# Kernel tuning notes

Hardware: AMD Instinct MI355X
Metric: run time of the kernel (lower is better)

Reference implementation:

```python
import jax, jax.numpy as jnp
import numpy as np


def setup_inputs() -> dict:
    key = jax.random.key(0)
    k_x, k_pos, k_val, k_temp = jax.random.split(key, 4)
    B, T, D, N = 8, 2048, 512, 4096
    x = jax.random.normal(k_x, (B, T, D), dtype=jnp.float32)
    # module init: positions ~ N(0,1)*0.5, values ~ N(0,1)*0.02
    positions = jax.random.normal(k_pos, (N, D), dtype=jnp.float32) * 0.5
    values = jax.random.normal(k_val, (N, D), dtype=jnp.float32) * 0.02
    # 'trained' temperatures ~ U[4,6] so the RBF kernel does not underflow at D=512
    temperature = 4.0 + 2.0 * jax.random.uniform(k_temp, (N,), dtype=jnp.float32)
    # neuron_scale buffer at late-tide level (MAX_SCALE = 0.8)
    neuron_scale = jnp.full((N,), 0.8, dtype=jnp.float32)
    return {"x": x, "positions": positions, "values": values,
            "temperature": temperature, "neuron_scale": neuron_scale}


def reference(x, positions, values, temperature, neuron_scale):
    B, T, D = x.shape
    x_flat = x.reshape(-1, D)                                  # [M, D], M = B*T
    x_sq = jnp.sum(x_flat * x_flat, axis=-1, keepdims=True)    # [M, 1]
    p_sq = jnp.sum(positions * positions, axis=-1)             # [N]
    cross = x_flat @ positions.T                               # [M, N] GEMM
    dists = jnp.sqrt(jnp.maximum(x_sq + p_sq[None, :] - 2.0 * cross, 0.0))
    effective_temp = (jnp.abs(temperature) + 0.1) * neuron_scale  # [N]
    weights = jnp.exp(-dists / effective_temp[None, :])        # [M, N]
    weights = weights / (jnp.sum(weights, axis=-1, keepdims=True) + 1e-8)
    out = weights @ values                                     # [M, D] GEMM
    return out.reshape(B, T, D)
```

## Files before the change

kernel.cpp:

```cpp
#include <hip/hip_runtime.h>
#include <hip/hip_bf16.h>

typedef __attribute__((ext_vector_type(8))) short short8;
typedef __attribute__((ext_vector_type(4))) float f32x4;
typedef __attribute__((ext_vector_type(4))) unsigned short u16x4;

__device__ __forceinline__ unsigned short f2bf(float f) {
  union { float f; unsigned u; } v; v.f = f;
  unsigned r = v.u + 0x7fffu + ((v.u >> 16) & 1u);
  return (unsigned short)(r >> 16);
}

template <int EPI, int WM, int WN, int MI, int BK, int NBUF>
__global__ __launch_bounds__(WM * WN * 64, 4) void rbf_gemm(
    const unsigned short* __restrict__ A, const unsigned short* __restrict__ Bt,
    int Ncols, int K,
    const float* __restrict__ xsq, const float* __restrict__ psq,
    const float* __restrict__ rtemp, unsigned short* __restrict__ Wout,
    float* __restrict__ part, int Mtot, const float* __restrict__ denin,
    float* __restrict__ outp, int row0, int ldOut) {
  constexpr int NT = WM * WN * 64;
  constexpr int BM = WM * MI * 16;
  constexpr int BN = WN * 64;
  constexpr int CH = BK / 8;
  constexpr int CMASK = CH - 1;
  constexpr int AIT = BM * CH / NT;
  constexpr int BIT = BN * CH / NT;
  constexpr int LOADS = AIT + BIT;
  constexpr int KS = BK / 32;
  constexpr int ASZ = BM * BK;
  constexpr int TSZ = (BM + BN) * BK;
  constexpr int BOUNCE = EPI == 1 ? BM * BN * 2 : BM * BN;
  constexpr int SELEMS = NBUF * TSZ > BOUNCE ? NBUF * TSZ : BOUNCE;
  __shared__ __align__(16) unsigned short smem[SELEMS];

  const int t = threadIdx.x;
  const int lane = t & 63, wid = t >> 6;
  const int wm = wid / WN, wn = wid % WN;
  const int lr = lane & 15, lg = lane >> 4;

  const int nbm = gridDim.x / (Ncols / BN);
  const int bm = blockIdx.x % nbm;
  const int bn = blockIdx.x / nbm;

  const unsigned short* Ab = A + (size_t)bm * BM * K;
  const unsigned short* Bb = Bt + (size_t)bn * BN * K;

  const unsigned short* gA[AIT];
  const unsigned short* gB[BIT];
#pragma unroll
  for (int i = 0; i < AIT; ++i) {
    const int idx = i * NT + t;
    const int r = idx / CH, c = idx & CMASK;
    gA[i] = Ab + (size_t)r * K + ((c ^ (r & CMASK)) << 3);
  }
#pragma unroll
  for (int i = 0; i < BIT; ++i) {
    const int idx = i * NT + t;
    const int r = idx / CH, c = idx & CMASK;
    gB[i] = Bb + (size_t)r * K + ((c ^ (r & CMASK)) << 3);
  }
  const int dwave = wid << 9;

  int offA[MI][KS], offB[4][KS];
#pragma unroll
  for (int mi = 0; mi < MI; ++mi) {
    const int ar = wm * (MI * 16) + mi * 16 + lr;
#pragma unroll
    for (int ks = 0; ks < KS; ++ks)
      offA[mi][ks] = ar * BK + ((((ks << 2) | lg) ^ (ar & CMASK)) << 3);
  }
#pragma unroll
  for (int ni = 0; ni < 4; ++ni) {
    const int br = wn * 64 + ni * 16 + lr;
#pragma unroll
    for (int ks = 0; ks < KS; ++ks)
      offB[ni][ks] = ASZ + br * BK + ((((ks << 2) | lg) ^ (br & CMASK)) << 3);
  }

  f32x4 acc[MI][4];
#pragma unroll
  for (int i = 0; i < MI; ++i)
#pragma unroll
    for (int j = 0; j < 4; ++j) acc[i][j] = (f32x4){0.f, 0.f, 0.f, 0.f};

#define STAGE(bo)                                                                      \
  do {                                                                                 \
    _Pragma("unroll")                                                                  \
    for (int i = 0; i < AIT; ++i) {                                                    \
      __builtin_amdgcn_global_load_lds(                                                \
          (const __attribute__((address_space(1))) void*)gA[i],                        \
          (__attribute__((address_space(3))) void*)(smem + (bo) + i * (NT * 8) + dwave), \
          16, 0, 0);                                                                   \
      gA[i] += BK;                                                                     \
    }                                                                                  \
    _Pragma("unroll")                                                                  \
    for (int i = 0; i < BIT; ++i) {                                                    \
      __builtin_amdgcn_global_load_lds(                                                \
          (const __attribute__((address_space(1))) void*)gB[i],                        \
          (__attribute__((address_space(3))) void*)(smem + (bo) + ASZ + i * (NT * 8) + dwave), \
          16, 0, 0);                                                                   \
      gB[i] += BK;                                                                     \
    }                                                                                  \
  } while (0)

  const int nsteps = K / BK;
  STAGE(0);
  unsigned buf = 0;
  for (int s = 0; s < nsteps; ++s) {
    if (s + 1 < nsteps) {
      STAGE(buf ^ TSZ);
      asm volatile("s_waitcnt vmcnt(%0)" :: "i"(LOADS) : "memory");
    } else {
      asm volatile("s_waitcnt vmcnt(0)" ::: "memory");
    }
    __builtin_amdgcn_s_barrier();
    const unsigned short* sb = smem + buf;
    __builtin_amdgcn_s_setprio(1);
#pragma unroll
    for (int ks = 0; ks < KS; ++ks) {
      short8 af[MI], bf[4];
#pragma unroll
      for (int mi = 0; mi < MI; ++mi) af[mi] = *(const short8*)&sb[offA[mi][ks]];
#pragma unroll
      for (int ni = 0; ni < 4; ++ni) bf[ni] = *(const short8*)&sb[offB[ni][ks]];
#pragma unroll
      for (int mi = 0; mi < MI; ++mi)
#pragma unroll
        for (int ni = 0; ni < 4; ++ni)
          acc[mi][ni] = __builtin_amdgcn_mfma_f32_16x16x32_bf16(af[mi], bf[ni],
                                                                acc[mi][ni], 0, 0, 0);
    }
    __builtin_amdgcn_s_setprio(0);
    asm volatile("s_waitcnt lgkmcnt(0)" ::: "memory");
    __builtin_amdgcn_s_barrier();
    buf ^= TSZ;
  }
#undef STAGE

  if (EPI == 0) {
    float ps[4], rt[4];
#pragma unroll
    for (int ni = 0; ni < 4; ++ni) {
      const int col = bn * BN + wn * 64 + ni * 16 + lr;
      ps[ni] = psq[col];
      rt[ni] = rtemp[col];
    }
    float* slice = part + (size_t)(bn * WN + wn) * Mtot;
#pragma unroll
    for (int mi = 0; mi < MI; ++mi) {
#pragma unroll
      for (int j = 0; j < 4; ++j) {
        const int lrow = wm * (MI * 16) + mi * 16 + lg * 4 + j;
        const int grow = row0 + bm * BM + lrow;
        const float xq = xsq[grow];
        float rsv = 0.f;
#pragma unroll
        for (int ni = 0; ni < 4; ++ni) {
          const int lcol = wn * 64 + ni * 16 + lr;
          float d2 = xq + ps[ni] - 2.0f * acc[mi][ni][j];
          float dist = __builtin_amdgcn_sqrtf(fmaxf(d2, 0.0f));
          float w = __builtin_amdgcn_exp2f(-dist * rt[ni]);
          smem[lrow * BN + (((lcol >> 3) ^ (lrow & 7)) << 3) + (lcol & 7)] = f2bf(w);
          rsv += w;
        }
        rsv += __shfl_xor(rsv, 1);
        rsv += __shfl_xor(rsv, 2);
        rsv += __shfl_xor(rsv, 4);
        rsv += __shfl_xor(rsv, 8);
        if (lr == 0) slice[grow] = rsv;
      }
    }
    __syncthreads();
    constexpr int HB = BN / 8;
#pragma unroll
    for (int i = 0; i < BM * BN / 8 / NT; ++i) {
      const int id = i * NT + t;
      const int r = id / HB, h = id % HB;
      short8 v = *(const short8*)&smem[r * BN + ((h ^ (r & 7)) << 3)];
      *(short8*)&Wout[(size_t)(bm * BM + r) * ldOut + bn * BN + h * 8] = v;
    }
  } else {
    float* smemf = (float*)smem;
#pragma unroll
    for (int mi = 0; mi < MI; ++mi)
#pragma unroll
      for (int j = 0; j < 4; ++j) {
        const int lrow = wm * (MI * 16) + mi * 16 + lg * 4 + j;
#pragma unroll
        for (int ni = 0; ni < 4; ++ni) {
          const int lcol = wn * 64 + ni * 16 + lr;
          smemf[lrow * BN + (((lcol >> 2) ^ (lrow & 7)) << 2) + (lcol & 3)] =
              acc[mi][ni][j];
        }
      }
    __syncthreads();
    constexpr int HB4 = BN / 4;
#pragma unroll
    for (int i = 0; i < BM * BN / 4 / NT; ++i) {
      const int id = i * NT + t;
      const int r = id / HB4, h = id % HB4;
      const int grow = row0 + bm * BM + r;
      const float rd = 1.0f / (denin[grow] + 1e-8f);
      f32x4 v = *(const f32x4*)&smemf[r * BN + ((h ^ (r & 7)) << 2)];
      v *= rd;
      __builtin_nontemporal_store(v,
          (f32x4*)&outp[(size_t)grow * ldOut + bn * BN + h * 4]);
    }
  }
}

__global__ void reduce_denom(const float* __restrict__ part, float* __restrict__ denom,
                             int Mtot, int row0, int S) {
  const int m = row0 + blockIdx.x * 128 + threadIdx.x;
  float s = 0.f;
  for (int i = 0; i < S; ++i) s += part[(size_t)i * Mtot + m];
  denom[m] = s;
}

__global__ void prep_rows(const float* __restrict__ in, unsigned short* __restrict__ outb,
                          float* __restrict__ sq, int D) {
  const int row = blockIdx.x;
  const int t = threadIdx.x;
  const float4 v = ((const float4*)(in + (size_t)row * D))[t];
  u16x4 o = {f2bf(v.x), f2bf(v.y), f2bf(v.z), f2bf(v.w)};
  *(u16x4*)(outb + (size_t)row * D + t * 4) = o;
  float s = v.x * v.x + v.y * v.y + v.z * v.z + v.w * v.w;
  for (int off = 32; off; off >>= 1) s += __shfl_xor(s, off);
  __shared__ float ws[16];
  if ((t & 63) == 0) ws[t >> 6] = s;
  __syncthreads();
  if (t == 0) {
    float tot = 0.f;
    const int nw = blockDim.x >> 6;
    for (int i = 0; i < nw; ++i) tot += ws[i];
    sq[row] = tot;
  }
}

__global__ void prep_scale(const float* __restrict__ tmp, const float* __restrict__ sc,
                           float* __restrict__ rtemp, int N) {
  const int i = blockIdx.x * blockDim.x + threadIdx.x;
  if (i < N) rtemp[i] = 1.4426950408889634f / ((fabsf(tmp[i]) + 0.1f) * sc[i]);
}

__global__ void prep_vT(const float* __restrict__ vals, unsigned short* __restrict__ vT,
                        int N, int D) {
  __shared__ float tile[32][33];
  const int nt = blockIdx.x, dt = blockIdx.y;
  const int tx = threadIdx.x, ty = threadIdx.y;
#pragma unroll
  for (int i = 0; i < 4; ++i) {
    int r = nt * 32 + ty + i * 8;
    tile[ty + i * 8][tx] = vals[(size_t)r * D + dt * 32 + tx];
  }
  __syncthreads();
#pragma unroll
  for (int i = 0; i < 4; ++i) {
    int d = dt * 32 + ty + i * 8;
    vT[(size_t)d * N + nt * 32 + tx] = f2bf(tile[tx][ty + i * 8]);
  }
}

extern "C" void kernel_launch(void* const* d_in, const int* in_sizes, int n_in,
                              void* d_out, int out_size, void* d_ws, size_t ws_size,
                              hipStream_t stream) {
  const float* x = (const float*)d_in[0];
  const float* pos = (const float*)d_in[1];
  const float* vals = (const float*)d_in[2];
  const float* temp = (const float*)d_in[3];
  const float* nsc = (const float*)d_in[4];
  float* out = (float*)d_out;

  const int N = in_sizes[3];
  const int D = in_sizes[1] / N;
  const int M = in_sizes[0] / D;
  const int S = 2 * (N / 128);

  char* ws = (char*)d_ws;
  size_t off = 0;
  auto alloc = [&](size_t bytes) {
    void* p = ws + off;
    off = (off + bytes + 255) & ~(size_t)255;
    return p;
  };
  unsigned short* xb = (unsigned short*)alloc((size_t)M * D * 2);
  unsigned short* pb = (unsigned short*)alloc((size_t)N * D * 2);
  unsigned short* vT = (unsigned short*)alloc((size_t)D * N * 2);
  float* xsq = (float*)alloc((size_t)M * 4);
  float* psq = (float*)alloc((size_t)N * 4);
  float* rtemp = (float*)alloc((size_t)N * 4);
  float* denom = (float*)alloc((size_t)M * 4);
  float* part = (float*)alloc((size_t)S * M * 4);

  size_t avail = ws_size > off ? ws_size - off : 0;
  long long mc_ll = (long long)(avail / ((size_t)N * 2));
  int Mc = (int)((mc_ll / 128) * 128);
  if (Mc > M) Mc = M;
  if (Mc < 128) Mc = 128;
  unsigned short* W = (unsigned short*)alloc((size_t)Mc * N * 2);

  prep_rows<<<M, D / 4, 0, stream>>>(x, xb, xsq, D);
  prep_rows<<<N, D / 4, 0, stream>>>(pos, pb, psq, D);
  prep_scale<<<(N + 255) / 256, 256, 0, stream>>>(temp, nsc, rtemp, N);
  dim3 tg(N / 32, D / 32);
  prep_vT<<<tg, dim3(32, 8), 0, stream>>>(vals, vT, N, D);

  for (int row0 = 0; row0 < M; row0 += Mc) {
    const int mc = (M - row0) < Mc ? (M - row0) : Mc;
    const int g1 = (mc / 128) * (N / 128);
    rbf_gemm<0, 4, 2, 2, 64, 2><<<g1, 512, 0, stream>>>(
        xb + (size_t)row0 * D, pb, N, D, xsq, psq, rtemp, W, part, M,
        nullptr, nullptr, row0, N);
    reduce_denom<<<mc / 128, 128, 0, stream>>>(part, denom, M, row0, S);
    const int g2 = (mc / 128) * (D / 256);
    rbf_gemm<1, 2, 4, 4, 64, 2><<<g2, 512, 0, stream>>>(
        W, vT, D, N, nullptr, nullptr, nullptr, nullptr,
        part, M, denom, out, row0, D);
  }
}
```

Measured before the change: 210.3 us.

## Replace first GEMM with 256x256-tile kernel using phased load/MFMA interleave

Adds a dedicated first-GEMM kernel with 256x256 output tiles, 8 waves and a four-phase schedule. Each phase interleaves LDS fragment reads, partial global-to-LDS prefetch of the next K-slice, barriers and MFMA blocks. The larger tile raises arithmetic intensity and the phased prefetch is meant to hide load latency behind MFMA work. In exchange it uses more registers and LDS, which lowers occupancy to 2 blocks per CU and produces fewer, larger blocks. The denominator-partial count and chunk granularity are adjusted to match.

```diff
diff --git a/kernel.cpp b/kernel.cpp
--- a/kernel.cpp
+++ b/kernel.cpp
@@ -11,13 +11,227 @@
   return (unsigned short)(r >> 16);
 }
 
-template <int EPI, int WM, int WN, int MI, int BK, int NBUF>
-__global__ __launch_bounds__(WM * WN * 64, 4) void rbf_gemm(
+#define GLL(src, dst)                                                     \
+  __builtin_amdgcn_global_load_lds(                                       \
+      (const __attribute__((address_space(1))) void*)(src),               \
+      (__attribute__((address_space(3))) void*)(dst), 16, 0, 0)
+#define BAR __builtin_amdgcn_s_barrier()
+#define LGKM0                                                             \
+  do {                                                                    \
+    asm volatile("s_waitcnt lgkmcnt(0)" ::: "memory");                    \
+    __builtin_amdgcn_sched_barrier(0);                                    \
+  } while (0)
+#define VMC(n) asm volatile("s_waitcnt vmcnt(" #n ")" ::: "memory")
+
+__global__ __launch_bounds__(512, 2) void rbf_qk8p(
     const unsigned short* __restrict__ A, const unsigned short* __restrict__ Bt,
     int Ncols, int K,
     const float* __restrict__ xsq, const float* __restrict__ psq,
     const float* __restrict__ rtemp, unsigned short* __restrict__ Wout,
-    float* __restrict__ part, int Mtot, const float* __restrict__ denin,
+    float* __restrict__ part, int Mtot, int row0, int ldOut) {
+  constexpr int BK = 64;
+  constexpr int ASZ = 256 * 64;
+  constexpr int TSZ = 512 * 64;
+  __shared__ __align__(16) unsigned short smem[2 * TSZ];
+
+  const int t = threadIdx.x;
+  const int lane = t & 63, wid = t >> 6;
+  const int wm = wid >> 2, wn = wid & 3;
+  const int lr = lane & 15, lg = lane >> 4;
+
+  const int nbm = gridDim.x / (Ncols >> 8);
+  const int bm = blockIdx.x % nbm;
+  const int bn = blockIdx.x / nbm;
+
+  const unsigned short* Ab = A + (size_t)bm * 256 * K;
+  const unsigned short* Bb = Bt + (size_t)bn * 256 * K;
+
+  const unsigned short* gB[4];
+#pragma unroll
+  for (int h = 0; h < 2; ++h)
+#pragma unroll
+    for (int i = 0; i < 2; ++i) {
+      const int idx = i * 512 + t;
+      const int r = h * 128 + (idx >> 3), c = idx & 7;
+      gB[h * 2 + i] = Bb + (size_t)r * K + ((c ^ (r & 7)) << 3);
+    }
+  const unsigned short* gAq[4];
+  {
+    const int half = t >> 8, rl = (t & 255) >> 3, c = t & 7;
+#pragma unroll
+    for (int q = 0; q < 4; ++q) {
+      const int R = half * 128 + q * 32 + rl;
+      gAq[q] = Ab + (size_t)R * K + ((c ^ (R & 7)) << 3);
+    }
+  }
+  const int dwB = wid << 9;
+  const int abase = ((wid >> 2) << 13) + ((wid & 3) << 9);
+
+#define STB(bo)                                         \
+  do {                                                  \
+    GLL(gB[0], smem + (bo) + ASZ + dwB);                \
+    gB[0] += BK;                                        \
+    GLL(gB[1], smem + (bo) + ASZ + 4096 + dwB);         \
+    gB[1] += BK;                                        \
+    GLL(gB[2], smem + (bo) + ASZ + 8192 + dwB);         \
+    gB[2] += BK;                                        \
+    GLL(gB[3], smem + (bo) + ASZ + 12288 + dwB);        \
+    gB[3] += BK;                                        \
+  } while (0)
+#define STA(bo, q)                                      \
+  do {                                                  \
+    GLL(gAq[q], smem + (bo) + abase + (q) * 2048);      \
+    gAq[q] += BK;                                       \
+  } while (0)
+
+  int offA[8][2], offB[4][2];
+#pragma unroll
+  for (int mi = 0; mi < 8; ++mi) {
+    const int ar = wm * 128 + mi * 16 + lr;
+#pragma unroll
+    for (int ks = 0; ks < 2; ++ks)
+      offA[mi][ks] = ar * 64 + ((((ks << 2) | lg) ^ (ar & 7)) << 3);
+  }
+#pragma unroll
+  for (int ni = 0; ni < 4; ++ni) {
+    const int br = wn * 64 + ni * 16 + lr;
+#pragma unroll
+    for (int ks = 0; ks < 2; ++ks)
+      offB[ni][ks] = ASZ + br * 64 + ((((ks << 2) | lg) ^ (br & 7)) << 3);
+  }
+
+  f32x4 acc[8][4];
+#pragma unroll
+  for (int i = 0; i < 8; ++i)
+#pragma unroll
+    for (int j = 0; j < 4; ++j) acc[i][j] = (f32x4){0.f, 0.f, 0.f, 0.f};
+
+#define PH_READS_A(p)                                   \
+  afr[0][0] = *(const short8*)&sb[offA[2 * (p)][0]];    \
+  afr[0][1] = *(const short8*)&sb[offA[2 * (p)][1]];    \
+  afr[1][0] = *(const short8*)&sb[offA[2 * (p) + 1][0]]; \
+  afr[1][1] = *(const short8*)&sb[offA[2 * (p) + 1][1]];
+#define PH_MFMA(p)                                                            \
+  __builtin_amdgcn_s_setprio(1);                                              \
+  _Pragma("unroll") for (int ks = 0; ks < 2; ++ks)                            \
+  _Pragma("unroll") for (int r = 0; r < 2; ++r)                               \
+  _Pragma("unroll") for (int ni = 0; ni < 4; ++ni)                            \
+      acc[2 * (p) + r][ni] = __builtin_amdgcn_mfma_f32_16x16x32_bf16(         \
+          afr[r][ks], bfr[ni][ks], acc[2 * (p) + r][ni], 0, 0, 0);            \
+  __builtin_amdgcn_s_setprio(0);
+
+  const int nsteps = K / BK;
+  const int last = nsteps - 1;
+  STB(0);
+  STA(0, 0);
+  STA(0, 1);
+  STA(0, 2);
+  STA(0, 3);
+  VMC(2);
+  BAR;
+
+  for (int tt = 0; tt < nsteps; ++tt) {
+    const int bo = (tt & 1) * TSZ, nbo = bo ^ TSZ;
+    const bool st = tt + 1 < nsteps;
+    const unsigned short* sb = smem + bo;
+    short8 bfr[4][2], afr[2][2];
+#pragma unroll
+    for (int ni = 0; ni < 4; ++ni) {
+      bfr[ni][0] = *(const short8*)&sb[offB[ni][0]];
+      bfr[ni][1] = *(const short8*)&sb[offB[ni][1]];
+    }
+    PH_READS_A(0)
+    if (st) STB(nbo);
+    BAR;
+    LGKM0;
+    PH_MFMA(0)
+    BAR;
+    PH_READS_A(1)
+    if (st) {
+      STA(nbo, 0);
+      STA(nbo, 1);
+    }
+    BAR;
+    LGKM0;
+    PH_MFMA(1)
+    if (tt == last) {
+      VMC(1);
+    } else {
+      VMC(7);
+    }
+    BAR;
+    PH_READS_A(2)
+    if (st) STA(nbo, 2);
+    BAR;
+    LGKM0;
+    PH_MFMA(2)
+    if (tt == last) {
+      VMC(0);
+    } else {
+      VMC(7);
+    }
+    BAR;
+    PH_READS_A(3)
+    if (st) STA(nbo, 3);
+    BAR;
+    LGKM0;
+    PH_MFMA(3)
+    if (tt != last) {
+      VMC(2);
+    }
+    BAR;
+  }
+#undef PH_READS_A
+#undef PH_MFMA
+#undef STB
+#undef STA
+
+  float ps[4], rt[4];
+#pragma unroll
+  for (int ni = 0; ni < 4; ++ni) {
+    const int col = bn * 256 + wn * 64 + ni * 16 + lr;
+    ps[ni] = psq[col];
+    rt[ni] = rtemp[col];
+  }
+  float* slice = part + (size_t)(bn * 4 + wn) * Mtot;
+#pragma unroll
+  for (int mi = 0; mi < 8; ++mi) {
+#pragma unroll
+    for (int j = 0; j < 4; ++j) {
+      const int lrow = wm * 128 + mi * 16 + lg * 4 + j;
+      const int grow = row0 + bm * 256 + lrow;
+      const float xq = xsq[grow];
+      float rsv = 0.f;
+#pragma unroll
+      for (int ni = 0; ni < 4; ++ni) {
+        const int lcol = wn * 64 + ni * 16 + lr;
+        float d2 = xq + ps[ni] - 2.0f * acc[mi][ni][j];
+        float dist = __builtin_amdgcn_sqrtf(fmaxf(d2, 0.0f));
+        float w = __builtin_amdgcn_exp2f(-dist * rt[ni]);
+        smem[lrow * 256 + (((lcol >> 3) ^ (lrow & 7)) << 3) + (lcol & 7)] = f2bf(w);
+        rsv += w;
+      }
+      rsv += __shfl_xor(rsv, 1);
+      rsv += __shfl_xor(rsv, 2);
+      rsv += __shfl_xor(rsv, 4);
+      rsv += __shfl_xor(rsv, 8);
+      if (lr == 0) slice[grow] = rsv;
+    }
+  }
+  __syncthreads();
+#pragma unroll
+  for (int i = 0; i < 16; ++i) {
+    const int id = i * 512 + t;
+    const int r = id >> 5, h = id & 31;
+    short8 v = *(const short8*)&smem[r * 256 + ((h ^ (r & 7)) << 3)];
+    *(short8*)&Wout[(size_t)(bm * 256 + r) * ldOut + bn * 256 + h * 8] = v;
+  }
+}
+
+template <int EPI, int WM, int WN, int MI, int BK, int NBUF>
+__global__ __launch_bounds__(WM * WN * 64, 4) void rbf_gemm(
+    const unsigned short* __restrict__ A, const unsigned short* __restrict__ Bt,
+    int Ncols, int K, const float* __restrict__ denin,
     float* __restrict__ outp, int row0, int ldOut) {
   constexpr int NT = WM * WN * 64;
   constexpr int BM = WM * MI * 16;
@@ -30,7 +244,7 @@
   constexpr int KS = BK / 32;
   constexpr int ASZ = BM * BK;
   constexpr int TSZ = (BM + BN) * BK;
-  constexpr int BOUNCE = EPI == 1 ? BM * BN * 2 : BM * BN;
+  constexpr int BOUNCE = BM * BN * 2;
   constexpr int SELEMS = NBUF * TSZ > BOUNCE ? NBUF * TSZ : BOUNCE;
   __shared__ __align__(16) unsigned short smem[SELEMS];
 
@@ -84,24 +298,16 @@
 #pragma unroll
     for (int j = 0; j < 4; ++j) acc[i][j] = (f32x4){0.f, 0.f, 0.f, 0.f};
 
-#define STAGE(bo)                                                                      \
-  do {                                                                                 \
-    _Pragma("unroll")                                                                  \
-    for (int i = 0; i < AIT; ++i) {                                                    \
-      __builtin_amdgcn_global_load_lds(                                                \
-          (const __attribute__((address_space(1))) void*)gA[i],                        \
-          (__attribute__((address_space(3))) void*)(smem + (bo) + i * (NT * 8) + dwave), \
-          16, 0, 0);                                                                   \
-      gA[i] += BK;                                                                     \
-    }                                                                                  \
-    _Pragma("unroll")                                                                  \
-    for (int i = 0; i < BIT; ++i) {                                                    \
-      __builtin_amdgcn_global_load_lds(                                                \
-          (const __attribute__((address_space(1))) void*)gB[i],                        \
-          (__attribute__((address_space(3))) void*)(smem + (bo) + ASZ + i * (NT * 8) + dwave), \
-          16, 0, 0);                                                                   \
-      gB[i] += BK;                                                                     \
-    }                                                                                  \
+#define STAGE(bo)                                                              \
+  do {                                                                         \
+    _Pragma("unroll") for (int i = 0; i < AIT; ++i) {                          \
+      GLL(gA[i], smem + (bo) + i * (NT * 8) + dwave);                          \
+      gA[i] += BK;                                                             \
+    }                                                                          \
+    _Pragma("unroll") for (int i = 0; i < BIT; ++i) {                          \
+      GLL(gB[i], smem + (bo) + ASZ + i * (NT * 8) + dwave);                    \
+      gB[i] += BK;                                                             \
+    }                                                                          \
   } while (0)
 
   const int nsteps = K / BK;
@@ -114,7 +320,7 @@
     } else {
       asm volatile("s_waitcnt vmcnt(0)" ::: "memory");
     }
-    __builtin_amdgcn_s_barrier();
+    BAR;
     const unsigned short* sb = smem + buf;
     __builtin_amdgcn_s_setprio(1);
 #pragma unroll
@@ -133,80 +339,36 @@
     }
     __builtin_amdgcn_s_setprio(0);
     asm volatile("s_waitcnt lgkmcnt(0)" ::: "memory");
-    __builtin_amdgcn_s_barrier();
+    BAR;
     buf ^= TSZ;
   }
 #undef STAGE
 
-  if (EPI == 0) {
-    float ps[4], rt[4];
-#pragma unroll
-    for (int ni = 0; ni < 4; ++ni) {
-      const int col = bn * BN + wn * 64 + ni * 16 + lr;
-      ps[ni] = psq[col];
-      rt[ni] = rtemp[col];
-    }
-    float* slice = part + (size_t)(bn * WN + wn) * Mtot;
-#pragma unroll
-    for (int mi = 0; mi < MI; ++mi) {
-#pragma unroll
-      for (int j = 0; j < 4; ++j) {
-        const int lrow = wm * (MI * 16) + mi * 16 + lg * 4 + j;
-        const int grow = row0 + bm * BM + lrow;
-        const float xq = xsq[grow];
-        float rsv = 0.f;
-#pragma unroll
-        for (int ni = 0; ni < 4; ++ni) {
-          const int lcol = wn * 64 + ni * 16 + lr;
-          float d2 = xq + ps[ni] - 2.0f * acc[mi][ni][j];
-          float dist = __builtin_amdgcn_sqrtf(fmaxf(d2, 0.0f));
-          float w = __builtin_amdgcn_exp2f(-dist * rt[ni]);
-          smem[lrow * BN + (((lcol >> 3) ^ (lrow & 7)) << 3) + (lcol & 7)] = f2bf(w);
-          rsv += w;
-        }
-        rsv += __shfl_xor(rsv, 1);
-        rsv += __shfl_xor(rsv, 2);
-        rsv += __shfl_xor(rsv, 4);
-        rsv += __shfl_xor(rsv, 8);
-        if (lr == 0) slice[grow] = rsv;
+  float* smemf = (float*)smem;
+#pragma unroll
+  for (int mi = 0; mi < MI; ++mi)
+#pragma unroll
+    for (int j = 0; j < 4; ++j) {
+      const int lrow = wm * (MI * 16) + mi * 16 + lg * 4 + j;
+#pragma unroll
+      for (int ni = 0; ni < 4; ++ni) {
+        const int lcol = wn * 64 + ni * 16 + lr;
+        smemf[lrow * BN + (((lcol >> 2) ^ (lrow & 7)) << 2) + (lcol & 3)] =
+            acc[mi][ni][j];
       }
     }
-    __syncthreads();
-    constexpr int HB = BN / 8;
-#pragma unroll
-    for (int i = 0; i < BM * BN / 8 / NT; ++i) {
-      const int id = i * NT + t;
-      const int r = id / HB, h = id % HB;
-      short8 v = *(const short8*)&smem[r * BN + ((h ^ (r & 7)) << 3)];
-      *(short8*)&Wout[(size_t)(bm * BM + r) * ldOut + bn * BN + h * 8] = v;
-    }
-  } else {
-    float* smemf = (float*)smem;
-#pragma unroll
-    for (int mi = 0; mi < MI; ++mi)
-#pragma unroll
-      for (int j = 0; j < 4; ++j) {
-        const int lrow = wm * (MI * 16) + mi * 16 + lg * 4 + j;
-#pragma unroll
-        for (int ni = 0; ni < 4; ++ni) {
-          const int lcol = wn * 64 + ni * 16 + lr;
-          smemf[lrow * BN + (((lcol >> 2) ^ (lrow & 7)) << 2) + (lcol & 3)] =
-              acc[mi][ni][j];
-        }
-      }
-    __syncthreads();
-    constexpr int HB4 = BN / 4;
-#pragma unroll
-    for (int i = 0; i < BM * BN / 4 / NT; ++i) {
-      const int id = i * NT + t;
-      const int r = id / HB4, h = id % HB4;
-      const int grow = row0 + bm * BM + r;
-      const float rd = 1.0f / (denin[grow] + 1e-8f);
-      f32x4 v = *(const f32x4*)&smemf[r * BN + ((h ^ (r & 7)) << 2)];
-      v *= rd;
-      __builtin_nontemporal_store(v,
-          (f32x4*)&outp[(size_t)grow * ldOut + bn * BN + h * 4]);
-    }
+  __syncthreads();
+  constexpr int HB4 = BN / 4;
+#pragma unroll
+  for (int i = 0; i < BM * BN / 4 / NT; ++i) {
+    const int id = i * NT + t;
+    const int r = id / HB4, h = id % HB4;
+    const int grow = row0 + bm * BM + r;
+    const float rd = 1.0f / (denin[grow] + 1e-8f);
+    f32x4 v = *(const f32x4*)&smemf[r * BN + ((h ^ (r & 7)) << 2)];
+    v *= rd;
+    __builtin_nontemporal_store(v,
+        (f32x4*)&outp[(size_t)grow * ldOut + bn * BN + h * 4]);
   }
 }
 
@@ -275,7 +437,7 @@
   const int N = in_sizes[3];
   const int D = in_sizes[1] / N;
   const int M = in_sizes[0] / D;
-  const int S = 2 * (N / 128);
+  const int S = 4 * (N / 256);
 
   char* ws = (char*)d_ws;
   size_t off = 0;
@@ -295,9 +457,9 @@
 
   size_t avail = ws_size > off ? ws_size - off : 0;
   long long mc_ll = (long long)(avail / ((size_t)N * 2));
-  int Mc = (int)((mc_ll / 128) * 128);
+  int Mc = (int)((mc_ll / 256) * 256);
   if (Mc > M) Mc = M;
-  if (Mc < 128) Mc = 128;
+  if (Mc < 256) Mc = 256;
   unsigned short* W = (unsigned short*)alloc((size_t)Mc * N * 2);
 
   prep_rows<<<M, D / 4, 0, stream>>>(x, xb, xsq, D);
@@ -308,14 +470,12 @@
 
   for (int row0 = 0; row0 < M; row0 += Mc) {
     const int mc = (M - row0) < Mc ? (M - row0) : Mc;
-    const int g1 = (mc / 128) * (N / 128);
-    rbf_gemm<0, 4, 2, 2, 64, 2><<<g1, 512, 0, stream>>>(
-        xb + (size_t)row0 * D, pb, N, D, xsq, psq, rtemp, W, part, M,
-        nullptr, nullptr, row0, N);
+    const int g1 = (mc / 256) * (N / 256);
+    rbf_qk8p<<<g1, 512, 0, stream>>>(xb + (size_t)row0 * D, pb, N, D,
+                                     xsq, psq, rtemp, W, part, M, row0, N);
     reduce_denom<<<mc / 128, 128, 0, stream>>>(part, denom, M, row0, S);
     const int g2 = (mc / 128) * (D / 256);
     rbf_gemm<1, 2, 4, 4, 64, 2><<<g2, 512, 0, stream>>>(
-        W, vT, D, N, nullptr, nullptr, nullptr, nullptr,
-        part, M, denom, out, row0, D);
-  }
-}
+        W, vT, D, N, denom, out, row0, D);
+  }
+}
```

Result: slower. 220.9 us (+5.0%).
